# Kernel tuning notes

Hardware: AMD Instinct MI355X
Metric: run time of the kernel (lower is better)

The kernel has to match this reference:

```python
import jax, jax.numpy as jnp
import numpy as np

B, L, H, D, M = 4, 2048, 16, 64, 128
EPS = 1e-6


def _create_projection_matrix(key, m, d):
    nb_full_blocks = m // d
    keys = jax.random.split(key, nb_full_blocks + 2)
    blocks = []
    for i in range(nb_full_blocks):
        unstructured = jax.random.normal(keys[i], (d, d), dtype=jnp.float32)
        q, _ = jnp.linalg.qr(unstructured)
        blocks.append(q.T)
    remaining = m - nb_full_blocks * d
    if remaining > 0:
        unstructured = jax.random.normal(keys[nb_full_blocks], (d, d), dtype=jnp.float32)
        q, _ = jnp.linalg.qr(unstructured)
        blocks.append(q.T[:remaining])
    final = jnp.concatenate(blocks, axis=0)  # [m, d]
    multiplier = jnp.linalg.norm(jax.random.normal(keys[-1], (m, d), dtype=jnp.float32), axis=1)
    return multiplier[:, None] * final


def setup_inputs() -> dict:
    key = jax.random.key(0)
    kq, kk, kv, kp = jax.random.split(key, 4)
    return {
        "q": jax.random.normal(kq, (B, L, H, D), dtype=jnp.float32),
        "k": jax.random.normal(kk, (B, L, H, D), dtype=jnp.float32),
        "v": jax.random.normal(kv, (B, L, H, D), dtype=jnp.float32),
        "projection_matrix": _create_projection_matrix(kp, M, D),
    }


def _softmax_kernel(data, proj, is_query, eps=EPS):
    # data: [B,L,H,D], proj: [M,D]
    data = (data.shape[-1] ** -0.25) * data
    ratio = proj.shape[0] ** -0.5
    data_dash = jnp.einsum('blhd,md->blhm', data, proj)  # [B,L,H,M]
    diag = jnp.sum(data * data, axis=-1, keepdims=True) * 0.5  # [B,L,H,1]
    if is_query:
        mx = jnp.max(data_dash, axis=-1, keepdims=True)
    else:
        mx = jnp.max(data_dash, axis=(1, 3), keepdims=True)
    return ratio * (jnp.exp(data_dash - diag - mx) + eps)


def reference(q, k, v, projection_matrix):
    qp = _softmax_kernel(q, projection_matrix, True)   # [B,L,H,M]
    kp = _softmax_kernel(k, projection_matrix, False)  # [B,L,H,M]
    # move L to the front for the causal scan
    qs = jnp.swapaxes(qp, 0, 1)  # [L,B,H,M]
    ks = jnp.swapaxes(kp, 0, 1)  # [L,B,H,M]
    vs = jnp.swapaxes(v, 0, 1)   # [L,B,H,D]

    def step(carry, inp):
        s, dsum = carry                 # s: [B,H,M,D], dsum: [B,H,M]
        q_t, k_t, v_t = inp
        s = s + k_t[..., :, None] * v_t[..., None, :]  # outer product accumulate
        dsum = dsum + k_t
        num = jnp.einsum('bhmd,bhm->bhd', s, q_t)      # [B,H,D]
        den = jnp.einsum('bhm,bhm->bh', q_t, dsum)     # [B,H]
        return (s, dsum), (num, den)

    init = (jnp.zeros((qs.shape[1], qs.shape[2], qs.shape[3], vs.shape[3]), qs.dtype),
            jnp.zeros_like(ks[0]))
    _, (nums, dens) = jax.lax.scan(step, init, (qs, ks, vs))
    av = jnp.swapaxes(nums, 0, 1)          # [B,L,H,D]
    norm = jnp.swapaxes(dens, 0, 1)[..., None]  # [B,L,H,1]
    return av / norm
```

## Files before the change

kernel.cpp:

```cpp
#include <hip/hip_runtime.h>
#include <math.h>

#define B_ 4
#define L_ 2048
#define H_ 16
#define D_ 64
#define M_ 128
#define TC_ 64
#define NC_ (L_ / TC_)
#define EPSK 1e-6f
#define DATA_SCALE 0.35355339059327379f
#define RATIO 0.08838834764831845f

typedef __bf16 bf16;
typedef bf16 bf16x4 __attribute__((ext_vector_type(4)));
typedef bf16 bf16x8 __attribute__((ext_vector_type(8)));
typedef float floatx4 __attribute__((ext_vector_type(4)));

#define PK128 136
#define PK64 72

__device__ __forceinline__ unsigned pk(bf16 a, bf16 b) {
    return (unsigned)__builtin_bit_cast(unsigned short, a) |
           ((unsigned)__builtin_bit_cast(unsigned short, b) << 16);
}
__device__ __forceinline__ void split2(float x, bf16& hi, bf16& lo) {
    hi = (bf16)x;
    lo = (bf16)(x - (float)hi);
}

__device__ __forceinline__ unsigned enc_f(float f) {
    unsigned u = __float_as_uint(f);
    return (u & 0x80000000u) ? ~u : (u | 0x80000000u);
}
__device__ __forceinline__ float dec_f(unsigned u) {
    unsigned b = (u & 0x80000000u) ? (u ^ 0x80000000u) : ~u;
    return __uint_as_float(b);
}

__global__ __launch_bounds__(256) void proj_split(const float* __restrict__ proj,
                                                  bf16* __restrict__ pfh,
                                                  bf16* __restrict__ pfl,
                                                  unsigned* __restrict__ mx) {
    int f = blockIdx.x * 256 + threadIdx.x;
    if (blockIdx.x == 0 && threadIdx.x < B_ * H_) mx[threadIdx.x] = 0u;
    int tc = f >> 7, k0h = (f >> 6) & 1, lane = f & 63;
    int lr = lane & 15, quad = lane >> 4;
    const float* src = proj + (16 * tc + lr) * 64 + k0h * 32 + quad * 8;
    float4 x0 = *(const float4*)src;
    float4 x1 = *(const float4*)(src + 4);
    float a[8] = {x0.x, x0.y, x0.z, x0.w, x1.x, x1.y, x1.z, x1.w};
    bf16x8 hi, lo;
#pragma unroll
    for (int e = 0; e < 8; e++) {
        bf16 h = (bf16)a[e];
        hi[e] = h;
        lo[e] = (bf16)(a[e] - (float)h);
    }
    *(bf16x8*)(pfh + (size_t)f * 8) = hi;
    *(bf16x8*)(pfl + (size_t)f * 8) = lo;
}

template <int MODE>
__global__ __launch_bounds__(256) void feat_mfma(const float* __restrict__ data,
                                                 const bf16* __restrict__ pfh,
                                                 const bf16* __restrict__ pfl,
                                                 unsigned* __restrict__ mxk,
                                                 bf16* __restrict__ outp,
                                                 bf16* __restrict__ outT) {
    __shared__ __align__(16) bf16 sc[64 * 130];
    __shared__ float wred[4];

    int tid = threadIdx.x;
    int blk = blockIdx.x;
    int c = blk & 31, h = (blk >> 5) & 15, b = blk >> 9;
    int l0 = c * 64;
    int w = tid >> 6, lane = tid & 63, lr = lane & 15, quad = lane >> 4;

    const float* drow = data +
        ((size_t)(b * L_ + l0 + 16 * w + lr) * H_ + h) * D_ + quad * 8;
    bf16x8 ah[2], al[2];
    float ss = 0.f;
#pragma unroll
    for (int k0 = 0; k0 < 2; k0++) {
        float4 x0 = *(const float4*)(drow + k0 * 32);
        float4 x1 = *(const float4*)(drow + k0 * 32 + 4);
        float a[8] = {x0.x, x0.y, x0.z, x0.w, x1.x, x1.y, x1.z, x1.w};
#pragma unroll
        for (int e = 0; e < 8; e++) {
            float s = DATA_SCALE * a[e];
            if (MODE != 0) ss += s * s;
            bf16 hh = (bf16)s;
            ah[k0][e] = hh;
            if (MODE != 0) al[k0][e] = (bf16)(s - (float)hh);
        }
    }
    float ssrow = 0.f;
    if (MODE != 0) {
        ss += __shfl_xor(ss, 16, 64);
        ss += __shfl_xor(ss, 32, 64);
        ssrow = 0.5f * ss;
    }

    floatx4 acc[8];
#pragma unroll
    for (int tc = 0; tc < 8; tc++) acc[tc] = (floatx4){0.f, 0.f, 0.f, 0.f};

    const bf16x8* ph = (const bf16x8*)pfh + lane;
    const bf16x8* pl = (const bf16x8*)pfl + lane;
#pragma unroll
    for (int tc = 0; tc < 8; tc++) {
#pragma unroll
        for (int k0 = 0; k0 < 2; k0++) {
            bf16x8 bh = ph[(tc * 2 + k0) * 64];
            acc[tc] = __builtin_amdgcn_mfma_f32_16x16x32_bf16(ah[k0], bh, acc[tc], 0, 0, 0);
            if (MODE != 0) {
                bf16x8 bl = pl[(tc * 2 + k0) * 64];
                acc[tc] = __builtin_amdgcn_mfma_f32_16x16x32_bf16(al[k0], bh, acc[tc], 0, 0, 0);
                acc[tc] = __builtin_amdgcn_mfma_f32_16x16x32_bf16(ah[k0], bl, acc[tc], 0, 0, 0);
            }
        }
    }

    if (MODE == 0) {
        float mm = acc[0][0];
#pragma unroll
        for (int tc = 0; tc < 8; tc++)
#pragma unroll
            for (int reg = 0; reg < 4; reg++) mm = fmaxf(mm, acc[tc][reg]);
#pragma unroll
        for (int off = 1; off < 64; off <<= 1) mm = fmaxf(mm, __shfl_xor(mm, off, 64));
        if (lane == 0) wred[w] = mm;
        __syncthreads();
        if (tid == 0) {
            float g = fmaxf(fmaxf(wred[0], wred[1]), fmaxf(wred[2], wred[3]));
            atomicMax(&mxk[b * H_ + h], enc_f(g));
        }
        return;
    }

    int t0 = 16 * w + 4 * quad;
    float mxg = 0.f;
    if (MODE == 1) mxg = dec_f(mxk[b * H_ + h]);

    float rm[4];
    if (MODE == 2) {
#pragma unroll
        for (int reg = 0; reg < 4; reg++) {
            float m = acc[0][reg];
#pragma unroll
            for (int tc = 1; tc < 8; tc++) m = fmaxf(m, acc[tc][reg]);
            m = fmaxf(m, __shfl_xor(m, 1, 64));
            m = fmaxf(m, __shfl_xor(m, 2, 64));
            m = fmaxf(m, __shfl_xor(m, 4, 64));
            m = fmaxf(m, __shfl_xor(m, 8, 64));
            rm[reg] = m;
        }
    }

#pragma unroll
    for (int reg = 0; reg < 4; reg++) {
        float dg = __shfl(ssrow, 4 * quad + reg, 64);
        float sh = (MODE == 1) ? (dg + mxg) : (dg + rm[reg]);
#pragma unroll
        for (int tc = 0; tc < 8; tc++) {
            float val = RATIO * (__expf(acc[tc][reg] - sh) + EPSK);
            sc[(t0 + reg) * 130 + 16 * tc + lr] = (bf16)val;
        }
    }
    __syncthreads();

#pragma unroll
    for (int i = 0; i < 16; i++) {
        int e = tid + 256 * i;
        int row = e >> 6, mp = e & 63;
        unsigned u = pk(sc[row * 130 + 2 * mp], sc[row * 130 + 2 * mp + 1]);
        *(unsigned*)(outp + ((size_t)(b * L_ + l0 + row) * H_ + h) * M_ + 2 * mp) = u;
    }
    if (MODE == 1) {
#pragma unroll
        for (int i = 0; i < 16; i++) {
            int e = tid + 256 * i;
            int m = e >> 5, t2 = (e & 31) * 2;
            unsigned u = pk(sc[t2 * 130 + m], sc[(t2 + 1) * 130 + m]);
            *(unsigned*)(outT + ((size_t)(b * H_ + h) * M_ + m) * L_ + l0 + t2) = u;
        }
    }
}

__global__ __launch_bounds__(256) void v_tr(const float* __restrict__ v,
                                            bf16* __restrict__ vbT) {
    __shared__ __align__(16) bf16 vt[64 * 66];
    int tid = threadIdx.x;
    int blk = blockIdx.x;
    int c = blk & 31, hh = (blk >> 5) & 15, b = blk >> 9;
#pragma unroll
    for (int i = 0; i < 4; i++) {
        int ch = tid + 256 * i;
        int row = ch >> 4, c4 = ch & 15;
        size_t gb = ((size_t)(b * L_ + c * 64 + row) * H_ + hh) * D_;
        float4 x = *(const float4*)(v + gb + c4 * 4);
        unsigned* lp = (unsigned*)(vt + row * 66 + c4 * 4);
        lp[0] = pk((bf16)x.x, (bf16)x.y);
        lp[1] = pk((bf16)x.z, (bf16)x.w);
    }
    __syncthreads();
    size_t ob = (size_t)((b * H_ + hh) * D_) * (size_t)L_ + c * 64;
#pragma unroll
    for (int i = 0; i < 8; i++) {
        int e2 = tid + 256 * i;
        int d = e2 >> 5, tau2 = (e2 & 31) * 2;
        *(unsigned*)(vbT + ob + (size_t)d * L_ + tau2) =
            pk(vt[tau2 * 66 + d], vt[(tau2 + 1) * 66 + d]);
    }
}

__global__ __launch_bounds__(256) void chunk_mfma(const bf16* __restrict__ kpT,
                                                  const bf16* __restrict__ vbT,
                                                  bf16* __restrict__ S,
                                                  float* __restrict__ ds) {
    __shared__ __align__(16) bf16 kT[128 * PK64];
    __shared__ __align__(16) bf16 vT[64 * PK64];
    int tid = threadIdx.x;
    int blk = blockIdx.x;
    int c = blk & 31, bh = blk >> 5;
    int l0 = c * 64;
#pragma unroll
    for (int i = 0; i < 4; i++) {
        int ch = tid + 256 * i;
        int m = ch >> 3, c8 = ch & 7;
        *(uint4*)(kT + m * PK64 + c8 * 8) =
            ((const uint4*)kpT)[(((size_t)bh * M_ + m) * L_ + l0) / 8 + c8];
    }
#pragma unroll
    for (int i = 0; i < 2; i++) {
        int ch = tid + 256 * i;
        int d = ch >> 3, c8 = ch & 7;
        *(uint4*)(vT + d * PK64 + c8 * 8) =
            ((const uint4*)vbT)[(((size_t)bh * D_ + d) * L_ + l0) / 8 + c8];
    }
    __syncthreads();

    int w = tid >> 6, lane = tid & 63, lr = lane & 15, quad = lane >> 4;
    floatx4 acc[8];
#pragma unroll
    for (int tc = 0; tc < 8; tc++) acc[tc] = (floatx4){0.f, 0.f, 0.f, 0.f};
#pragma unroll
    for (int k0 = 0; k0 < 64; k0 += 32) {
        bf16x8 a = *(const bf16x8*)(vT + (16 * w + lr) * PK64 + k0 + quad * 8);
#pragma unroll
        for (int tc = 0; tc < 8; tc++) {
            bf16x8 bb = *(const bf16x8*)(kT + (16 * tc + lr) * PK64 + k0 + quad * 8);
            acc[tc] = __builtin_amdgcn_mfma_f32_16x16x32_bf16(a, bb, acc[tc], 0, 0, 0);
        }
    }

    float dsv = 0.f;
    {
        int m = tid >> 1, half = tid & 1;
        const bf16x8* kr = (const bf16x8*)(kT + m * PK64 + half * 32);
#pragma unroll
        for (int j = 0; j < 4; j++) {
            bf16x8 vv = kr[j];
#pragma unroll
            for (int e = 0; e < 8; e++) dsv += (float)vv[e];
        }
        dsv += __shfl_xor(dsv, 1, 64);
    }
    __syncthreads();

    bf16* scr = kT;
    int d0 = 16 * w + 4 * quad;
#pragma unroll
    for (int tc = 0; tc < 8; tc++)
#pragma unroll
        for (int reg = 0; reg < 4; reg++)
            scr[(d0 + reg) * 128 + 16 * tc + lr] = (bf16)acc[tc][reg];
    if ((tid & 1) == 0) ds[(size_t)blk * M_ + (tid >> 1)] = dsv;
    __syncthreads();
#pragma unroll
    for (int i = 0; i < 4; i++) {
        int e = tid + 256 * i;
        ((uint4*)S)[(size_t)blk * 1024 + e] = ((const uint4*)scr)[e];
    }
}

__global__ void prefix_S(unsigned* __restrict__ S) {
    int blk = blockIdx.x;
    int seg = blk & 15, bh = blk >> 4;
    int p = seg * 256 + threadIdx.x;
    size_t base = (size_t)bh * NC_ * 4096 + p;
    float c0 = 0.f, c1 = 0.f;
    for (int c = 0; c < NC_; c++) {
        size_t a = base + (size_t)c * 4096;
        unsigned u = S[a];
        float f0 = (float)__builtin_bit_cast(bf16, (unsigned short)(u & 0xffffu));
        float f1 = (float)__builtin_bit_cast(bf16, (unsigned short)(u >> 16));
        S[a] = pk((bf16)c0, (bf16)c1);
        c0 += f0; c1 += f1;
    }
}

__global__ void prefix_D(float* __restrict__ ds) {
    int bh = blockIdx.x;
    int m = threadIdx.x;
    size_t base = (size_t)bh * NC_ * M_ + m;
    float carry = 0.f;
    for (int c = 0; c < NC_; c++) {
        size_t a = base + (size_t)c * M_;
        float val = ds[a];
        ds[a] = carry;
        carry += val;
    }
}

__global__ __launch_bounds__(256) void attn_mfma(const bf16* __restrict__ qp,
                                                 const bf16* __restrict__ kp,
                                                 const bf16* __restrict__ vbT,
                                                 const bf16* __restrict__ Sp,
                                                 const float* __restrict__ dp,
                                                 float* __restrict__ out) {
    __shared__ __align__(16) bf16 arena[64 * PK128 * 2 + 64 * PK64];
    bf16* ks  = arena;
    bf16* spT = arena + 64 * PK128;
    bf16* sc  = spT;
    bf16* vT  = arena + 2 * 64 * PK128;
    __shared__ float dprevL[128];
    __shared__ float den0_l[64];
    __shared__ float densc_l[64];

    int tid = threadIdx.x;
    int blk = blockIdx.x;
    int c = blk & 31, bh = blk >> 5;
    int h = bh & 15, b = bh >> 4;
    int l0 = c * 64;

#pragma unroll
    for (int i = 0; i < 4; i++) {
        int ch = tid + 256 * i;
        int row = ch >> 4, c8 = ch & 15;
        size_t gb = (((size_t)(b * L_ + l0 + row) * H_ + h) * M_) / 8;
        *(uint4*)(ks + row * PK128 + c8 * 8) = ((const uint4*)kp)[gb + c8];
    }
#pragma unroll
    for (int i = 0; i < 4; i++) {
        int ch = tid + 256 * i;
        int row = ch >> 4, c8 = ch & 15;
        *(uint4*)(spT + row * PK128 + c8 * 8) = ((const uint4*)Sp)[(size_t)blk * 1024 + ch];
    }
#pragma unroll
    for (int i = 0; i < 2; i++) {
        int ch = tid + 256 * i;
        int d = ch >> 3, c8 = ch & 7;
        *(uint4*)(vT + d * PK64 + c8 * 8) =
            ((const uint4*)vbT)[(((size_t)bh * D_ + d) * L_ + l0) / 8 + c8];
    }
    if (tid < 128) dprevL[tid] = dp[(size_t)blk * M_ + tid];
    __syncthreads();

    {
        int t = tid >> 2, p = tid & 3;
        const bf16* qrow = qp + ((size_t)(b * L_ + l0 + t) * H_ + h) * M_ + p * 32;
        float s = 0.f;
#pragma unroll
        for (int j = 0; j < 4; j++) {
            bf16x8 vv = *(const bf16x8*)(qrow + 8 * j);
#pragma unroll
            for (int e = 0; e < 8; e++) s += (float)vv[e] * dprevL[p * 32 + 8 * j + e];
        }
        s += __shfl_xor(s, 1, 64);
        s += __shfl_xor(s, 2, 64);
        if (p == 0) den0_l[t] = s;
    }

    int w = tid >> 6, lane = tid & 63, lr = lane & 15, quad = lane >> 4;

    bf16x8 af[4];
    {
        const bf16* qb = qp + ((size_t)(b * L_ + l0 + 16 * w + lr) * H_ + h) * M_ + quad * 8;
#pragma unroll
        for (int k = 0; k < 4; k++) af[k] = *(const bf16x8*)(qb + 32 * k);
    }

    floatx4 acc[4];
#pragma unroll
    for (int tc = 0; tc < 4; tc++) acc[tc] = (floatx4){0.f, 0.f, 0.f, 0.f};

#pragma unroll
    for (int ki = 0; ki < 4; ki++) {
#pragma unroll
        for (int tc = 0; tc < 4; tc++) {
            bf16x8 bb = *(const bf16x8*)(spT + (16 * tc + lr) * PK128 + 32 * ki + quad * 8);
            acc[tc] = __builtin_amdgcn_mfma_f32_16x16x32_bf16(af[ki], bb, acc[tc], 0, 0, 0);
        }
    }

    floatx4 acc2[4];
#pragma unroll
    for (int tc = 0; tc < 4; tc++) acc2[tc] = (floatx4){0.f, 0.f, 0.f, 0.f};
#pragma unroll
    for (int ki = 0; ki < 4; ki++) {
        for (int tc = 0; tc <= w; tc++) {
            bf16x8 bb = *(const bf16x8*)(ks + (16 * tc + lr) * PK128 + 32 * ki + quad * 8);
            acc2[tc] = __builtin_amdgcn_mfma_f32_16x16x32_bf16(af[ki], bb, acc2[tc], 0, 0, 0);
        }
    }
    __syncthreads();

    {
        float dsum[4] = {0.f, 0.f, 0.f, 0.f};
        int t0 = 16 * w + 4 * quad;
#pragma unroll
        for (int tc = 0; tc < 4; tc++) {
#pragma unroll
            for (int reg = 0; reg < 4; reg++) {
                int tg = t0 + reg, tau = 16 * tc + lr;
                float vv = (tc <= w) ? acc2[tc][reg] : 0.f;
                if (tau > tg) vv = 0.f;
                dsum[reg] += vv;
                sc[tg * PK64 + tau] = (bf16)vv;
            }
        }
#pragma unroll
        for (int reg = 0; reg < 4; reg++) {
            float s = dsum[reg];
            s += __shfl_xor(s, 1, 64);
            s += __shfl_xor(s, 2, 64);
            s += __shfl_xor(s, 4, 64);
            s += __shfl_xor(s, 8, 64);
            if (lr == 0) densc_l[t0 + reg] = s;
        }
    }
    __syncthreads();

    {
        int kmax = (w >= 2) ? 64 : 32;
        for (int k0 = 0; k0 < kmax; k0 += 32) {
            bf16x8 a = *(const bf16x8*)(sc + (16 * w + lr) * PK64 + k0 + quad * 8);
#pragma unroll
            for (int tc = 0; tc < 4; tc++) {
                bf16x8 bb = *(const bf16x8*)(vT + (16 * tc + lr) * PK64 + k0 + quad * 8);
                acc[tc] = __builtin_amdgcn_mfma_f32_16x16x32_bf16(a, bb, acc[tc], 0, 0, 0);
            }
        }
    }

    {
        int t0 = 16 * w + 4 * quad;
        float inv[4];
#pragma unroll
        for (int reg = 0; reg < 4; reg++)
            inv[reg] = 1.0f / (den0_l[t0 + reg] + densc_l[t0 + reg]);
#pragma unroll
        for (int tc = 0; tc < 4; tc++)
#pragma unroll
            for (int reg = 0; reg < 4; reg++)
                out[((size_t)(b * L_ + l0 + t0 + reg) * H_ + h) * D_ + 16 * tc + lr] =
                    acc[tc][reg] * inv[reg];
    }
}

extern "C" void kernel_launch(void* const* d_in, const int* in_sizes, int n_in,
                              void* d_out, int out_size, void* d_ws, size_t ws_size,
                              hipStream_t stream) {
    const float* q = (const float*)d_in[0];
    const float* k = (const float*)d_in[1];
    const float* v = (const float*)d_in[2];
    const float* proj = (const float*)d_in[3];
    float* out = (float*)d_out;
    char* W = (char*)d_ws;

    bf16* qp   = (bf16*)(W);
    bf16* kp   = (bf16*)(W + 33554432ull);
    bf16* kpT  = (bf16*)(W + 67108864ull);
    bf16* vbT  = (bf16*)(W + 100663296ull);
    bf16* S    = (bf16*)(W + 117440512ull);
    float* ds  = (float*)(W + 150994944ull);
    unsigned* mx = (unsigned*)(W + 152043520ull);
    bf16* pfh  = (bf16*)(W + 152043776ull);
    bf16* pfl  = (bf16*)(W + 152060160ull);

    hipLaunchKernelGGL(proj_split, dim3(4), dim3(256), 0, stream, proj, pfh, pfl, mx);
    hipLaunchKernelGGL((feat_mfma<0>), dim3(2048), dim3(256), 0, stream,
                       k, pfh, pfl, mx, (bf16*)nullptr, (bf16*)nullptr);
    hipLaunchKernelGGL((feat_mfma<1>), dim3(2048), dim3(256), 0, stream,
                       k, pfh, pfl, mx, kp, kpT);
    hipLaunchKernelGGL((feat_mfma<2>), dim3(2048), dim3(256), 0, stream,
                       q, pfh, pfl, mx, qp, (bf16*)nullptr);
    hipLaunchKernelGGL(v_tr, dim3(2048), dim3(256), 0, stream, v, vbT);
    hipLaunchKernelGGL(chunk_mfma, dim3(2048), dim3(256), 0, stream, kpT, vbT, S, ds);
    hipLaunchKernelGGL(prefix_S, dim3(1024), dim3(256), 0, stream, (unsigned*)S);
    hipLaunchKernelGGL(prefix_D, dim3(64), dim3(128), 0, stream, ds);
    hipLaunchKernelGGL(attn_mfma, dim3(2048), dim3(256), 0, stream,
                       qp, kp, vbT, S, ds, out);
}
```

Before: 247.9 us.

## Merge preprocessing and prefix kernels, read S/kp directly from global in attention

Fuses the q-feature, k-max, and v-transpose kernels into one launch, and merges the S and denominator prefix scans into one kernel that preloads all chunks into registers. The attention kernel stops staging S and kp through shared memory and loads MFMA operands straight from global. It also computes the inter-chunk denominator from the already loaded q fragments via shuffles, and adds an occupancy hint. This cuts launch count, LDS footprint and barriers, but adds uncoalesced global reads and register pressure.

Result: faster. 235.1 us (-5.2%).

```diff
diff --git a/kernel.cpp b/kernel.cpp
--- a/kernel.cpp
+++ b/kernel.cpp
@@ -23,10 +23,6 @@
 __device__ __forceinline__ unsigned pk(bf16 a, bf16 b) {
     return (unsigned)__builtin_bit_cast(unsigned short, a) |
            ((unsigned)__builtin_bit_cast(unsigned short, b) << 16);
-}
-__device__ __forceinline__ void split2(float x, bf16& hi, bf16& lo) {
-    hi = (bf16)x;
-    lo = (bf16)(x - (float)hi);
 }
 
 __device__ __forceinline__ unsigned enc_f(float f) {
@@ -62,17 +58,14 @@
 }
 
 template <int MODE>
-__global__ __launch_bounds__(256) void feat_mfma(const float* __restrict__ data,
-                                                 const bf16* __restrict__ pfh,
-                                                 const bf16* __restrict__ pfl,
-                                                 unsigned* __restrict__ mxk,
-                                                 bf16* __restrict__ outp,
-                                                 bf16* __restrict__ outT) {
-    __shared__ __align__(16) bf16 sc[64 * 130];
-    __shared__ float wred[4];
-
+__device__ __forceinline__ void feat_body(const float* __restrict__ data,
+                                          const bf16* __restrict__ pfh,
+                                          const bf16* __restrict__ pfl,
+                                          unsigned* __restrict__ mxk,
+                                          bf16* __restrict__ outp,
+                                          bf16* __restrict__ outT,
+                                          int blk, bf16* sc, float* wred) {
     int tid = threadIdx.x;
-    int blk = blockIdx.x;
     int c = blk & 31, h = (blk >> 5) & 15, b = blk >> 9;
     int l0 = c * 64;
     int w = tid >> 6, lane = tid & 63, lr = lane & 15, quad = lane >> 4;
@@ -188,11 +181,10 @@
     }
 }
 
-__global__ __launch_bounds__(256) void v_tr(const float* __restrict__ v,
-                                            bf16* __restrict__ vbT) {
-    __shared__ __align__(16) bf16 vt[64 * 66];
+__device__ __forceinline__ void vtr_body(const float* __restrict__ v,
+                                         bf16* __restrict__ vbT,
+                                         int blk, bf16* vt) {
     int tid = threadIdx.x;
-    int blk = blockIdx.x;
     int c = blk & 31, hh = (blk >> 5) & 15, b = blk >> 9;
 #pragma unroll
     for (int i = 0; i < 4; i++) {
@@ -213,6 +205,38 @@
         *(unsigned*)(vbT + ob + (size_t)d * L_ + tau2) =
             pk(vt[tau2 * 66 + d], vt[(tau2 + 1) * 66 + d]);
     }
+}
+
+__global__ __launch_bounds__(256) void pre3(const float* __restrict__ q,
+                                            const float* __restrict__ k,
+                                            const float* __restrict__ v,
+                                            const bf16* __restrict__ pfh,
+                                            const bf16* __restrict__ pfl,
+                                            unsigned* __restrict__ mxk,
+                                            bf16* __restrict__ qp,
+                                            bf16* __restrict__ vbT) {
+    __shared__ __align__(16) bf16 arena[64 * 130];
+    __shared__ float wred[4];
+    int blk = blockIdx.x;
+    if (blk < 2048) {
+        feat_body<2>(q, pfh, pfl, mxk, qp, (bf16*)nullptr, blk, arena, wred);
+    } else if (blk < 4096) {
+        feat_body<0>(k, pfh, pfl, mxk, (bf16*)nullptr, (bf16*)nullptr, blk - 2048,
+                     arena, wred);
+    } else {
+        vtr_body(v, vbT, blk - 4096, arena);
+    }
+}
+
+__global__ __launch_bounds__(256) void feat_k(const float* __restrict__ k,
+                                              const bf16* __restrict__ pfh,
+                                              const bf16* __restrict__ pfl,
+                                              unsigned* __restrict__ mxk,
+                                              bf16* __restrict__ kp,
+                                              bf16* __restrict__ kpT) {
+    __shared__ __align__(16) bf16 arena[64 * 130];
+    __shared__ float wred[4];
+    feat_body<1>(k, pfh, pfl, mxk, kp, kpT, blockIdx.x, arena, wred);
 }
 
 __global__ __launch_bounds__(256) void chunk_mfma(const bf16* __restrict__ kpT,
@@ -285,69 +309,55 @@
     }
 }
 
-__global__ void prefix_S(unsigned* __restrict__ S) {
+__global__ void prefix_SD(unsigned* __restrict__ S, float* __restrict__ ds) {
     int blk = blockIdx.x;
     int seg = blk & 15, bh = blk >> 4;
     int p = seg * 256 + threadIdx.x;
     size_t base = (size_t)bh * NC_ * 4096 + p;
+    unsigned uv[NC_];
+#pragma unroll
+    for (int c = 0; c < NC_; c++) uv[c] = S[base + (size_t)c * 4096];
     float c0 = 0.f, c1 = 0.f;
+#pragma unroll
     for (int c = 0; c < NC_; c++) {
-        size_t a = base + (size_t)c * 4096;
-        unsigned u = S[a];
+        unsigned u = uv[c];
         float f0 = (float)__builtin_bit_cast(bf16, (unsigned short)(u & 0xffffu));
         float f1 = (float)__builtin_bit_cast(bf16, (unsigned short)(u >> 16));
-        S[a] = pk((bf16)c0, (bf16)c1);
+        S[base + (size_t)c * 4096] = pk((bf16)c0, (bf16)c1);
         c0 += f0; c1 += f1;
     }
-}
-
-__global__ void prefix_D(float* __restrict__ ds) {
-    int bh = blockIdx.x;
-    int m = threadIdx.x;
-    size_t base = (size_t)bh * NC_ * M_ + m;
-    float carry = 0.f;
-    for (int c = 0; c < NC_; c++) {
-        size_t a = base + (size_t)c * M_;
-        float val = ds[a];
-        ds[a] = carry;
-        carry += val;
-    }
-}
-
-__global__ __launch_bounds__(256) void attn_mfma(const bf16* __restrict__ qp,
-                                                 const bf16* __restrict__ kp,
-                                                 const bf16* __restrict__ vbT,
-                                                 const bf16* __restrict__ Sp,
-                                                 const float* __restrict__ dp,
-                                                 float* __restrict__ out) {
-    __shared__ __align__(16) bf16 arena[64 * PK128 * 2 + 64 * PK64];
-    bf16* ks  = arena;
-    bf16* spT = arena + 64 * PK128;
-    bf16* sc  = spT;
-    bf16* vT  = arena + 2 * 64 * PK128;
+    if (seg == 0 && threadIdx.x < 128) {
+        int m = threadIdx.x;
+        size_t dbase = (size_t)bh * NC_ * M_ + m;
+        float dv[NC_];
+#pragma unroll
+        for (int c = 0; c < NC_; c++) dv[c] = ds[dbase + (size_t)c * M_];
+        float carry = 0.f;
+#pragma unroll
+        for (int c = 0; c < NC_; c++) {
+            ds[dbase + (size_t)c * M_] = carry;
+            carry += dv[c];
+        }
+    }
+}
+
+__global__ __launch_bounds__(256, 4) void attn_mfma(const bf16* __restrict__ qp,
+                                                    const bf16* __restrict__ kp,
+                                                    const bf16* __restrict__ vbT,
+                                                    const bf16* __restrict__ Sp,
+                                                    const float* __restrict__ dp,
+                                                    float* __restrict__ out) {
+    __shared__ __align__(16) bf16 vT[64 * PK64];
+    __shared__ __align__(16) bf16 sc[64 * PK64];
     __shared__ float dprevL[128];
-    __shared__ float den0_l[64];
-    __shared__ float densc_l[64];
 
     int tid = threadIdx.x;
     int blk = blockIdx.x;
     int c = blk & 31, bh = blk >> 5;
     int h = bh & 15, b = bh >> 4;
     int l0 = c * 64;
-
-#pragma unroll
-    for (int i = 0; i < 4; i++) {
-        int ch = tid + 256 * i;
-        int row = ch >> 4, c8 = ch & 15;
-        size_t gb = (((size_t)(b * L_ + l0 + row) * H_ + h) * M_) / 8;
-        *(uint4*)(ks + row * PK128 + c8 * 8) = ((const uint4*)kp)[gb + c8];
-    }
-#pragma unroll
-    for (int i = 0; i < 4; i++) {
-        int ch = tid + 256 * i;
-        int row = ch >> 4, c8 = ch & 15;
-        *(uint4*)(spT + row * PK128 + c8 * 8) = ((const uint4*)Sp)[(size_t)blk * 1024 + ch];
-    }
+    int w = tid >> 6, lane = tid & 63, lr = lane & 15, quad = lane >> 4;
+
 #pragma unroll
     for (int i = 0; i < 2; i++) {
         int ch = tid + 256 * i;
@@ -356,60 +366,58 @@
             ((const uint4*)vbT)[(((size_t)bh * D_ + d) * L_ + l0) / 8 + c8];
     }
     if (tid < 128) dprevL[tid] = dp[(size_t)blk * M_ + tid];
+
+    bf16x8 af[4];
+    {
+        const bf16* qb = qp + ((size_t)(b * L_ + l0 + 16 * w + lr) * H_ + h) * M_ + quad * 8;
+#pragma unroll
+        for (int k = 0; k < 4; k++) af[k] = *(const bf16x8*)(qb + 32 * k);
+    }
     __syncthreads();
 
-    {
-        int t = tid >> 2, p = tid & 3;
-        const bf16* qrow = qp + ((size_t)(b * L_ + l0 + t) * H_ + h) * M_ + p * 32;
-        float s = 0.f;
-#pragma unroll
-        for (int j = 0; j < 4; j++) {
-            bf16x8 vv = *(const bf16x8*)(qrow + 8 * j);
-#pragma unroll
-            for (int e = 0; e < 8; e++) s += (float)vv[e] * dprevL[p * 32 + 8 * j + e];
-        }
-        s += __shfl_xor(s, 1, 64);
-        s += __shfl_xor(s, 2, 64);
-        if (p == 0) den0_l[t] = s;
-    }
-
-    int w = tid >> 6, lane = tid & 63, lr = lane & 15, quad = lane >> 4;
-
-    bf16x8 af[4];
-    {
-        const bf16* qb = qp + ((size_t)(b * L_ + l0 + 16 * w + lr) * H_ + h) * M_ + quad * 8;
-#pragma unroll
-        for (int k = 0; k < 4; k++) af[k] = *(const bf16x8*)(qb + 32 * k);
-    }
+    float den0v = 0.f;
+#pragma unroll
+    for (int k = 0; k < 4; k++)
+#pragma unroll
+        for (int e = 0; e < 8; e++)
+            den0v += (float)af[k][e] * dprevL[quad * 8 + 32 * k + e];
+    den0v += __shfl_xor(den0v, 16, 64);
+    den0v += __shfl_xor(den0v, 32, 64);
 
     floatx4 acc[4];
 #pragma unroll
     for (int tc = 0; tc < 4; tc++) acc[tc] = (floatx4){0.f, 0.f, 0.f, 0.f};
 
-#pragma unroll
-    for (int ki = 0; ki < 4; ki++) {
-#pragma unroll
-        for (int tc = 0; tc < 4; tc++) {
-            bf16x8 bb = *(const bf16x8*)(spT + (16 * tc + lr) * PK128 + 32 * ki + quad * 8);
-            acc[tc] = __builtin_amdgcn_mfma_f32_16x16x32_bf16(af[ki], bb, acc[tc], 0, 0, 0);
+    {
+        const bf16* spb = Sp + (size_t)blk * 8192;
+#pragma unroll
+        for (int ki = 0; ki < 4; ki++) {
+#pragma unroll
+            for (int tc = 0; tc < 4; tc++) {
+                bf16x8 bb = *(const bf16x8*)(spb + (16 * tc + lr) * 128 + 32 * ki + quad * 8);
+                acc[tc] = __builtin_amdgcn_mfma_f32_16x16x32_bf16(af[ki], bb, acc[tc], 0, 0, 0);
+            }
         }
     }
 
     floatx4 acc2[4];
 #pragma unroll
     for (int tc = 0; tc < 4; tc++) acc2[tc] = (floatx4){0.f, 0.f, 0.f, 0.f};
-#pragma unroll
-    for (int ki = 0; ki < 4; ki++) {
-        for (int tc = 0; tc <= w; tc++) {
-            bf16x8 bb = *(const bf16x8*)(ks + (16 * tc + lr) * PK128 + 32 * ki + quad * 8);
-            acc2[tc] = __builtin_amdgcn_mfma_f32_16x16x32_bf16(af[ki], bb, acc2[tc], 0, 0, 0);
-        }
-    }
-    __syncthreads();
-
+    {
+        const bf16* kpb = kp + ((size_t)(b * L_ + l0) * H_ + h) * M_ + quad * 8;
+#pragma unroll
+        for (int ki = 0; ki < 4; ki++) {
+            for (int tc = 0; tc <= w; tc++) {
+                bf16x8 bb = *(const bf16x8*)(kpb + (size_t)(16 * tc + lr) * (H_ * M_) + 32 * ki);
+                acc2[tc] = __builtin_amdgcn_mfma_f32_16x16x32_bf16(af[ki], bb, acc2[tc], 0, 0, 0);
+            }
+        }
+    }
+
+    int t0 = 16 * w + 4 * quad;
+    float densc[4];
     {
         float dsum[4] = {0.f, 0.f, 0.f, 0.f};
-        int t0 = 16 * w + 4 * quad;
 #pragma unroll
         for (int tc = 0; tc < 4; tc++) {
 #pragma unroll
@@ -428,10 +436,9 @@
             s += __shfl_xor(s, 2, 64);
             s += __shfl_xor(s, 4, 64);
             s += __shfl_xor(s, 8, 64);
-            if (lr == 0) densc_l[t0 + reg] = s;
-        }
-    }
-    __syncthreads();
+            densc[reg] = s;
+        }
+    }
 
     {
         int kmax = (w >= 2) ? 64 : 32;
@@ -446,11 +453,12 @@
     }
 
     {
-        int t0 = 16 * w + 4 * quad;
         float inv[4];
 #pragma unroll
-        for (int reg = 0; reg < 4; reg++)
-            inv[reg] = 1.0f / (den0_l[t0 + reg] + densc_l[t0 + reg]);
+        for (int reg = 0; reg < 4; reg++) {
+            float d0 = __shfl(den0v, 4 * quad + reg, 64);
+            inv[reg] = 1.0f / (d0 + densc[reg]);
+        }
 #pragma unroll
         for (int tc = 0; tc < 4; tc++)
 #pragma unroll
@@ -481,16 +489,12 @@
     bf16* pfl  = (bf16*)(W + 152060160ull);
 
     hipLaunchKernelGGL(proj_split, dim3(4), dim3(256), 0, stream, proj, pfh, pfl, mx);
-    hipLaunchKernelGGL((feat_mfma<0>), dim3(2048), dim3(256), 0, stream,
-                       k, pfh, pfl, mx, (bf16*)nullptr, (bf16*)nullptr);
-    hipLaunchKernelGGL((feat_mfma<1>), dim3(2048), dim3(256), 0, stream,
+    hipLaunchKernelGGL(pre3, dim3(6144), dim3(256), 0, stream,
+                       q, k, v, pfh, pfl, mx, qp, vbT);
+    hipLaunchKernelGGL(feat_k, dim3(2048), dim3(256), 0, stream,
                        k, pfh, pfl, mx, kp, kpT);
-    hipLaunchKernelGGL((feat_mfma<2>), dim3(2048), dim3(256), 0, stream,
-                       q, pfh, pfl, mx, qp, (bf16*)nullptr);
-    hipLaunchKernelGGL(v_tr, dim3(2048), dim3(256), 0, stream, v, vbT);
     hipLaunchKernelGGL(chunk_mfma, dim3(2048), dim3(256), 0, stream, kpT, vbT, S, ds);
-    hipLaunchKernelGGL(prefix_S, dim3(1024), dim3(256), 0, stream, (unsigned*)S);
-    hipLaunchKernelGGL(prefix_D, dim3(64), dim3(128), 0, stream, ds);
+    hipLaunchKernelGGL(prefix_SD, dim3(1024), dim3(256), 0, stream, (unsigned*)S, ds);
     hipLaunchKernelGGL(attn_mfma, dim3(2048), dim3(256), 0, stream,
                        qp, kp, vbT, S, ds, out);
 }
```
